# Kernel optimization log

Hardware: AMD Instinct MI355X
Metric: run time of the kernel (lower is better)

## Reference

```python
import jax, jax.numpy as jnp
import numpy as np

DIM = 1024
HEADS = 16
HEAD_DIM = DIM // HEADS  # 64
B, T, S = 4, 2048, 2048
NEG = -1e9


def rotary_pos_emb(x, freqs):
    # x: (B, H, L, Dh), freqs: (L, Dh//2). Rotate interleaved (even, odd) pairs.
    cos = jnp.cos(freqs)[None, None, :, :]  # (1,1,L,Dh//2)
    sin = jnp.sin(freqs)[None, None, :, :]
    x_even = x[..., 0::2]
    x_odd = x[..., 1::2]
    r_even = x_even * cos - x_odd * sin
    r_odd = x_even * sin + x_odd * cos
    return jnp.stack([r_even, r_odd], axis=-1).reshape(x.shape)


def setup_inputs() -> dict:
    key = jax.random.key(0)
    ks = jax.random.split(key, 9)
    w_std = 1.0 / np.sqrt(DIM)
    return {
        "q_x": jax.random.normal(ks[0], (B, T, DIM), jnp.float32),
        "kv_x": jax.random.normal(ks[1], (B, S, DIM), jnp.float32),
        "freq_q": jax.random.normal(ks[2], (T, HEAD_DIM // 2), jnp.float32),
        "freq_kv": jax.random.normal(ks[3], (S, HEAD_DIM // 2), jnp.float32),
        "key_padding_mask": jax.random.randint(ks[4], (B, S), 0, 2, jnp.int32),
        "Wq": jax.random.normal(ks[5], (DIM, DIM), jnp.float32) * w_std,
        "Wk": jax.random.normal(ks[6], (DIM, DIM), jnp.float32) * w_std,
        "Wv": jax.random.normal(ks[7], (DIM, DIM), jnp.float32) * w_std,
        "Wproj": jax.random.normal(ks[8], (DIM, DIM), jnp.float32) * w_std,
    }


def reference(q_x, kv_x, freq_q, freq_kv, key_padding_mask, Wq, Wk, Wv, Wproj):
    b, t, d = q_x.shape
    s = kv_x.shape[1]
    # QKV projections (torch Linear: x @ W.T), split into heads -> (B, H, L, Dh)
    q = (q_x @ Wq.T).reshape(b, t, HEADS, HEAD_DIM).transpose(0, 2, 1, 3)
    k = (kv_x @ Wk.T).reshape(b, s, HEADS, HEAD_DIM).transpose(0, 2, 1, 3)
    v = (kv_x @ Wv.T).reshape(b, s, HEADS, HEAD_DIM).transpose(0, 2, 1, 3)
    # Rotary embedding on q and k
    q = rotary_pos_emb(q, freq_q)
    k = rotary_pos_emb(k, freq_kv)
    # Scaled dot-product attention with key-padding mask (True = attend)
    scale = HEAD_DIM ** (-0.5)
    scores = jnp.einsum('bhtd,bhsd->bhts', q, k) * scale
    mask = key_padding_mask.astype(bool)[:, None, None, :]  # (B,1,1,S)
    scores = jnp.where(mask, scores, NEG)
    attn = jax.nn.softmax(scores, axis=-1)
    out = jnp.einsum('bhts,bhsd->bhtd', attn, v)
    out = out.transpose(0, 2, 1, 3).reshape(b, t, d)
    return out @ Wproj.T
```

## Files before the change

### kernel.cpp

```cpp
#include <hip/hip_runtime.h>
#include <hip/hip_bf16.h>


typedef __bf16 bf16;
typedef __bf16 bf16x8 __attribute__((ext_vector_type(8)));
typedef __bf16 bf16x4 __attribute__((ext_vector_type(4)));
typedef float  f32x4  __attribute__((ext_vector_type(4)));

#define NB   4
#define NT   2048
#define NS   2048
#define NH   16
#define HD   64
#define SCL  0.18033688011112043f

__device__ __forceinline__ void gload16(const void* g, void* l) {
  __builtin_amdgcn_global_load_lds((const __attribute__((address_space(1))) void*)g,
                                   (__attribute__((address_space(3))) void*)l, 16, 0, 0);
}

__device__ __forceinline__ f32x4 mfma16(bf16x8 a, bf16x8 b, f32x4 c) {
  return __builtin_amdgcn_mfma_f32_16x16x32_bf16(a, b, c, 0, 0, 0);
}

__global__ void k_convert(const float* __restrict__ qx, const float* __restrict__ kvx,
                          const float* __restrict__ Wq, const float* __restrict__ Wk,
                          const float* __restrict__ Wv, const float* __restrict__ Wp,
                          bf16* __restrict__ wbf, bf16* __restrict__ qxbf,
                          bf16* __restrict__ kvxbf)
{
  const long total = 4194304L + 8388608L + 8388608L;
  for (long v = (long)blockIdx.x * blockDim.x + threadIdx.x; v * 4 < total;
       v += (long)gridDim.x * blockDim.x) {
    long e0 = v * 4;
    const float* src; bf16* dst;
    if (e0 < 4194304L) {
      int widx = (int)(e0 >> 20);
      const float* wsrc = (widx == 0) ? Wq : (widx == 1) ? Wk : (widx == 2) ? Wv : Wp;
      src = wsrc + (e0 & 1048575); dst = wbf + e0;
    } else if (e0 < 12582912L) {
      src = qx + (e0 - 4194304L); dst = qxbf + (e0 - 4194304L);
    } else {
      src = kvx + (e0 - 12582912L); dst = kvxbf + (e0 - 12582912L);
    }
    float4 f = *(const float4*)src;
    bf16x4 o = {(bf16)f.x, (bf16)f.y, (bf16)f.z, (bf16)f.w};
    *(bf16x4*)dst = o;
  }
}

__global__ void k_tables(const float* __restrict__ fq, const float* __restrict__ fkv,
                         const int* __restrict__ mask,
                         float2* __restrict__ csq, float2* __restrict__ cskv,
                         float* __restrict__ bias)
{
  int i = blockIdx.x * blockDim.x + threadIdx.x;
  if (i < 65536) {
    float s, c; sincosf(fq[i], &s, &c); csq[i] = make_float2(c, s);
  } else if (i < 131072) {
    int j = i - 65536;
    float s, c; sincosf(fkv[j], &s, &c); cskv[j] = make_float2(c, s);
  } else if (i < 139264) {
    int j = i - 131072;
    bias[j] = mask[j] ? 0.0f : -1.0e9f;
  }
}

template<int EPI>
__global__ __launch_bounds__(256) void k_gemm(
    const bf16* __restrict__ A0, const bf16* __restrict__ A1,
    const bf16* __restrict__ wbase,
    bf16* __restrict__ Qb, bf16* __restrict__ Kb, bf16* __restrict__ Vtb,
    float* __restrict__ Of,
    const float2* __restrict__ csq, const float2* __restrict__ cskv)
{
  __shared__ bf16 As[128 * 32];
  __shared__ bf16 Bs[128 * 32];
  const int z  = (EPI == 0) ? blockIdx.z : 0;
  const bf16* A = (EPI == 1) ? A0 : ((z == 0) ? A0 : A1);
  const bf16* W = wbase + (size_t)z * 1048576;
  const int m0 = blockIdx.x * 128, n0 = blockIdx.y * 128;
  const int tid = threadIdx.x, lane = tid & 63, w = tid >> 6;
  const int g = lane >> 4, c = lane & 15;
  const int wr = w >> 1, wc = w & 1;

  f32x4 acc[4][4];
#pragma unroll
  for (int i = 0; i < 4; ++i)
#pragma unroll
    for (int j = 0; j < 4; ++j) acc[i][j] = 0.0f;

  const bf16* gA = A + (size_t)(m0 + w * 32 + (lane >> 2)) * 1024 + (lane & 3) * 8;
  const bf16* gB = W + (size_t)(n0 + w * 32 + (lane >> 2)) * 1024 + (lane & 3) * 8;
  bf16* lA = As + w * 1024;
  bf16* lB = Bs + w * 1024;

  for (int k0 = 0; k0 < 1024; k0 += 32) {
    __syncthreads();
    gload16(gA, lA);               gload16(gA + 16 * 1024, lA + 512);
    gload16(gB, lB);               gload16(gB + 16 * 1024, lB + 512);
    gA += 32; gB += 32;
    __syncthreads();

    bf16x8 af[4], bfr[4];
#pragma unroll
    for (int mi = 0; mi < 4; ++mi)
      af[mi] = *(const bf16x8*)(As + (wr * 64 + mi * 16 + c) * 32 + g * 8);
#pragma unroll
    for (int ni = 0; ni < 4; ++ni)
      bfr[ni] = *(const bf16x8*)(Bs + (wc * 64 + ni * 16 + c) * 32 + g * 8);
#pragma unroll
    for (int mi = 0; mi < 4; ++mi)
#pragma unroll
      for (int ni = 0; ni < 4; ++ni)
        acc[mi][ni] = mfma16(af[mi], bfr[ni], acc[mi][ni]);
  }

  if (EPI == 1) {
#pragma unroll
    for (int mi = 0; mi < 4; ++mi)
#pragma unroll
      for (int ni = 0; ni < 4; ++ni)
#pragma unroll
        for (int r = 0; r < 4; ++r) {
          int m = m0 + wr * 64 + mi * 16 + g * 4 + r;
          int n = n0 + wc * 64 + ni * 16 + c;
          Of[(size_t)m * 1024 + n] = acc[mi][ni][r];
        }
  } else if (z < 2) {
    const float2* cs = (z == 0) ? csq : cskv;
    bf16* Out = (z == 0) ? Qb : Kb;
#pragma unroll
    for (int mi = 0; mi < 4; ++mi)
#pragma unroll
      for (int ni = 0; ni < 4; ++ni)
#pragma unroll
        for (int r = 0; r < 4; ++r) {
          int m = m0 + wr * 64 + mi * 16 + g * 4 + r;
          int n = n0 + wc * 64 + ni * 16 + c;
          float v = acc[mi][ni][r];
          float p = __shfl_xor(v, 1);
          int t = m & 2047, b = m >> 11;
          int h = n >> 6, d = n & 63;
          float2 cv = cs[t * 32 + (d >> 1)];
          float rot = (d & 1) ? (v * cv.x + p * cv.y)
                              : (v * cv.x - p * cv.y);
          Out[((size_t)((b * 16 + h) * 2048 + t)) * 64 + d] = (bf16)rot;
        }
  } else {
#pragma unroll
    for (int mi = 0; mi < 4; ++mi)
#pragma unroll
      for (int ni = 0; ni < 4; ++ni) {
        int m = m0 + wr * 64 + mi * 16 + g * 4;
        int n = n0 + wc * 64 + ni * 16 + c;
        int b = m >> 11, sl = m & 2047;
        int h = n >> 6, d = n & 63;
        int p  = sl & 63;
        int st = p >> 4, q4 = (p >> 2) & 3;
        int col = (sl & ~63) | ((st >> 1) << 5) | (q4 << 3) | ((st & 1) << 2);
        bf16x4 pk = {(bf16)acc[mi][ni][0], (bf16)acc[mi][ni][1],
                     (bf16)acc[mi][ni][2], (bf16)acc[mi][ni][3]};
        *(bf16x4*)(Vtb + ((size_t)((b * 16 + h) * 64 + d)) * 2048 + col) = pk;
      }
  }
}

__global__ __launch_bounds__(256) void k_attn(
    const bf16* __restrict__ Qb, const bf16* __restrict__ Kb,
    const bf16* __restrict__ Vtb, const float* __restrict__ bias,
    bf16* __restrict__ Ob)
{
  __shared__ bf16 Ks[2][64 * 64];
  __shared__ bf16 Vs[2][80 * 64];
  __shared__ float Bls[2048];
  const int bh = blockIdx.y, b = bh >> 4, h = bh & 15;
  const int t0 = blockIdx.x * 128;
  const int tid = threadIdx.x, lane = tid & 63, w = tid >> 6;
  const int g = lane >> 4, c = lane & 15;

  {
    int rr = tid >> 4;
    int col4 = (tid & 15) * 4;
    bf16 v = (rr == 0) ? (bf16)1.0f : (bf16)0.0f;
    bf16x4 vv = {v, v, v, v};
    *(bf16x4*)(&Vs[0][(64 + rr) * 64 + col4]) = vv;
    *(bf16x4*)(&Vs[1][(64 + rr) * 64 + col4]) = vv;
  }
  {
    const float* bsrc = bias + b * 2048;
    float4 b0 = *(const float4*)(bsrc + tid * 4);
    float4 b1 = *(const float4*)(bsrc + 1024 + tid * 4);
    *(float4*)(&Bls[tid * 4]) = b0;
    *(float4*)(&Bls[1024 + tid * 4]) = b1;
  }

  bf16x8 qf[2][2];
#pragma unroll
  for (int qt = 0; qt < 2; ++qt) {
    const bf16* qp = Qb + ((size_t)bh * 2048 + t0 + qt * 64 + w * 16 + c) * 64;
    qf[qt][0] = *(const bf16x8*)(qp + g * 8);
    qf[qt][1] = *(const bf16x8*)(qp + 32 + g * 8);
  }

  float mrun[2] = {-3.0e38f, -3.0e38f};
  f32x4 o[2][5];
#pragma unroll
  for (int qt = 0; qt < 2; ++qt)
#pragma unroll
    for (int ni = 0; ni < 5; ++ni) o[qt][ni] = 0.0f;

  const int srow8 = lane >> 3;
  const int scol  = ((lane & 7) ^ srow8) * 8;
  const bf16* gK = Kb  + ((size_t)bh * 2048 + w * 16 + srow8) * 64 + scol;
  const bf16* gV = Vtb + ((size_t)bh * 64 + w * 16 + srow8) * 2048 + scol;

#define STAGE(bufi, ti)  do {                                   \
    const bf16* k_ = gK + ((size_t)(ti) << 12);                 \
    const bf16* v_ = gV + (size_t)(ti) * 64;                    \
    bf16* lk_ = &Ks[bufi][w * 1024];                            \
    bf16* lv_ = &Vs[bufi][w * 1024];                            \
    gload16(k_, lk_);            gload16(k_ + 512,      lk_ + 512); \
    gload16(v_, lv_);            gload16(v_ + 8 * 2048, lv_ + 512); \
  } while (0)

  STAGE(0, 0);
  asm volatile("s_waitcnt vmcnt(0)" ::: "memory");
  __syncthreads();

  for (int ti = 0; ti < 32; ++ti) {
    const int cur = ti & 1;
    if (ti < 31) STAGE(cur ^ 1, ti + 1);

    const bf16* KsC = Ks[cur];
    const bf16* VsC = Vs[cur];

    f32x4 sc[2][4];
#pragma unroll
    for (int qt = 0; qt < 2; ++qt)
#pragma unroll
      for (int st = 0; st < 4; ++st) sc[qt][st] = 0.0f;
    __builtin_amdgcn_s_setprio(1);
#pragma unroll
    for (int kd = 0; kd < 2; ++kd)
#pragma unroll
      for (int st = 0; st < 4; ++st) {
        int srow = st * 16 + c;
        bf16x8 kf = *(const bf16x8*)(KsC + srow * 64 + ((kd * 4 + g) ^ (srow & 7)) * 8);
        sc[0][st] = mfma16(kf, qf[0][kd], sc[0][st]);
        sc[1][st] = mfma16(kf, qf[1][kd], sc[1][st]);
      }
    __builtin_amdgcn_s_setprio(0);

    float4 bv[4];
#pragma unroll
    for (int st = 0; st < 4; ++st)
      bv[st] = *(const float4*)(&Bls[ti * 64 + st * 16 + g * 4]);

    bf16x8 pf[2][2];
#pragma unroll
    for (int qt = 0; qt < 2; ++qt) {
      float sv[4][4];
#pragma unroll
      for (int st = 0; st < 4; ++st)
#pragma unroll
        for (int r = 0; r < 4; ++r)
          sv[st][r] = sc[qt][st][r] * SCL + ((const float*)&bv[st])[r];

      float mt = sv[0][0];
#pragma unroll
      for (int st = 0; st < 4; ++st)
#pragma unroll
        for (int r = 0; r < 4; ++r) mt = fmaxf(mt, sv[st][r]);
      mt = fmaxf(mt, __shfl_xor(mt, 16));
      mt = fmaxf(mt, __shfl_xor(mt, 32));

      if (__any(mt > mrun[qt] + 8.0f)) {
        float mnew = fmaxf(mrun[qt], mt);
        float corr = exp2f(mrun[qt] - mnew);
        mrun[qt] = mnew;
#pragma unroll
        for (int ni = 0; ni < 5; ++ni) o[qt][ni] *= corr;
      }
#pragma unroll
      for (int ks = 0; ks < 2; ++ks)
#pragma unroll
        for (int st2 = 0; st2 < 2; ++st2) {
          int st = ks * 2 + st2;
#pragma unroll
          for (int r = 0; r < 4; ++r)
            pf[qt][ks][st2 * 4 + r] = (bf16)exp2f(sv[st][r] - mrun[qt]);
        }
    }

    __builtin_amdgcn_s_setprio(1);
#pragma unroll
    for (int ks = 0; ks < 2; ++ks)
#pragma unroll
      for (int ni = 0; ni < 5; ++ni) {
        int vrow = ni * 16 + c;
        bf16x8 vf = *(const bf16x8*)(VsC + vrow * 64 + (((ks * 4 + g) ^ (vrow & 7)) * 8));
        o[0][ni] = mfma16(vf, pf[0][ks], o[0][ni]);
        o[1][ni] = mfma16(vf, pf[1][ks], o[1][ni]);
      }
    __builtin_amdgcn_s_setprio(0);

    asm volatile("s_waitcnt vmcnt(0) lgkmcnt(0)" ::: "memory");
    __builtin_amdgcn_s_barrier();
  }
#undef STAGE

#pragma unroll
  for (int qt = 0; qt < 2; ++qt) {
    float l = __shfl(o[qt][4][0], c);
    float rl = 1.0f / l;
    int t = t0 + qt * 64 + w * 16 + c;
#pragma unroll
    for (int ni = 0; ni < 4; ++ni) {
      bf16x4 ov = {(bf16)(o[qt][ni][0] * rl), (bf16)(o[qt][ni][1] * rl),
                   (bf16)(o[qt][ni][2] * rl), (bf16)(o[qt][ni][3] * rl)};
      *(bf16x4*)(Ob + ((size_t)(b * 2048 + t)) * 1024 + h * 64 + ni * 16 + g * 4) = ov;
    }
  }
}

extern "C" void kernel_launch(void* const* d_in, const int* in_sizes, int n_in,
                              void* d_out, int out_size, void* d_ws, size_t ws_size,
                              hipStream_t stream)
{
  const float* qx  = (const float*)d_in[0];
  const float* kvx = (const float*)d_in[1];
  const float* fq  = (const float*)d_in[2];
  const float* fkv = (const float*)d_in[3];
  const int*  mask = (const int*)  d_in[4];
  const float* Wq  = (const float*)d_in[5];
  const float* Wk  = (const float*)d_in[6];
  const float* Wv  = (const float*)d_in[7];
  const float* Wp  = (const float*)d_in[8];

  char* ws = (char*)d_ws;
  bf16*   wbf   = (bf16*)(ws);
  bf16*   qxbf  = (bf16*)(ws + 8388608);
  bf16*   kvxbf = (bf16*)(ws + 25165824);
  bf16*   Qb    = (bf16*)(ws + 41943040);
  bf16*   Kb    = (bf16*)(ws + 58720256);
  bf16*   Vtb   = (bf16*)(ws + 75497472);
  bf16*   Ob    = (bf16*)(ws + 92274688);
  float2* csq   = (float2*)(ws + 109051904);
  float2* cskv  = (float2*)(ws + 109576192);
  float*  bias  = (float*)(ws + 110100480);
  float*  out   = (float*)d_out;

  k_convert<<<4096, 256, 0, stream>>>(qx, kvx, Wq, Wk, Wv, Wp, wbf, qxbf, kvxbf);
  k_tables<<<544, 256, 0, stream>>>(fq, fkv, mask, csq, cskv, bias);
  k_gemm<0><<<dim3(64, 8, 3), 256, 0, stream>>>(qxbf, kvxbf, wbf,
                                                Qb, Kb, Vtb, nullptr, csq, cskv);
  k_attn<<<dim3(16, 64), 256, 0, stream>>>(Qb, Kb, Vtb, bias, Ob);
  k_gemm<1><<<dim3(64, 8, 1), 256, 0, stream>>>(Ob, nullptr, wbf + 3 * 1048576,
                                                nullptr, nullptr, nullptr, out, csq, cskv);
}
```

Measured before the change: 380.5 us.

## Overlap K/V prefetch in attention, shrink LDS with bf16 bias, remap blocks per XCD

The attention kernel now waits only for the current tile's loads (vmcnt(4)) and adds a barrier before compute, so the next tile's global-to-LDS prefetch stays in flight during the compute. It also stores the key-padding bias as bf16 and moves the ones-row used for the softmax denominator into a separate small LDS buffer, which cuts shared memory use and may allow more resident blocks. Block indices are remapped so blocks for the same batch-head land on the same XCD, aiming for better L2 reuse of K/V. The bf16 bias keeps 0 and about -1e9 close enough to their fp32 values, and the extra barrier per iteration adds some synchronisation cost.

```diff
diff --git a/kernel.cpp b/kernel.cpp
--- a/kernel.cpp
+++ b/kernel.cpp
@@ -52,7 +52,7 @@
 __global__ void k_tables(const float* __restrict__ fq, const float* __restrict__ fkv,
                          const int* __restrict__ mask,
                          float2* __restrict__ csq, float2* __restrict__ cskv,
-                         float* __restrict__ bias)
+                         float* __restrict__ bias, bf16* __restrict__ biasbf)
 {
   int i = blockIdx.x * blockDim.x + threadIdx.x;
   if (i < 65536) {
@@ -63,6 +63,9 @@
   } else if (i < 139264) {
     int j = i - 131072;
     bias[j] = mask[j] ? 0.0f : -1.0e9f;
+  } else if (i < 147456) {
+    int j = i - 139264;
+    biasbf[j] = mask[j] ? (bf16)0.0f : (bf16)(-1.0e9f);
   }
 }
 
@@ -168,14 +171,18 @@
 
 __global__ __launch_bounds__(256) void k_attn(
     const bf16* __restrict__ Qb, const bf16* __restrict__ Kb,
-    const bf16* __restrict__ Vtb, const float* __restrict__ bias,
+    const bf16* __restrict__ Vtb, const bf16* __restrict__ biasbf,
     bf16* __restrict__ Ob)
 {
   __shared__ bf16 Ks[2][64 * 64];
-  __shared__ bf16 Vs[2][80 * 64];
-  __shared__ float Bls[2048];
-  const int bh = blockIdx.y, b = bh >> 4, h = bh & 15;
-  const int t0 = blockIdx.x * 128;
+  __shared__ bf16 Vs[2][64 * 64];
+  __shared__ bf16 Vones[16 * 64];
+  __shared__ bf16 Blsb[2048];
+  const int lin = blockIdx.y * 16 + blockIdx.x;
+  const int xcd = lin & 7, j = lin >> 3;
+  const int bh = xcd * 8 + (j >> 4);
+  const int t0 = (j & 15) * 128;
+  const int b = bh >> 4, h = bh & 15;
   const int tid = threadIdx.x, lane = tid & 63, w = tid >> 6;
   const int g = lane >> 4, c = lane & 15;
 
@@ -184,16 +191,9 @@
     int col4 = (tid & 15) * 4;
     bf16 v = (rr == 0) ? (bf16)1.0f : (bf16)0.0f;
     bf16x4 vv = {v, v, v, v};
-    *(bf16x4*)(&Vs[0][(64 + rr) * 64 + col4]) = vv;
-    *(bf16x4*)(&Vs[1][(64 + rr) * 64 + col4]) = vv;
-  }
-  {
-    const float* bsrc = bias + b * 2048;
-    float4 b0 = *(const float4*)(bsrc + tid * 4);
-    float4 b1 = *(const float4*)(bsrc + 1024 + tid * 4);
-    *(float4*)(&Bls[tid * 4]) = b0;
-    *(float4*)(&Bls[1024 + tid * 4]) = b1;
-  }
+    *(bf16x4*)(&Vones[rr * 64 + col4]) = vv;
+  }
+  bf16x8 bb0 = *(const bf16x8*)(biasbf + b * 2048 + tid * 8);
 
   bf16x8 qf[2][2];
 #pragma unroll
@@ -202,6 +202,7 @@
     qf[qt][0] = *(const bf16x8*)(qp + g * 8);
     qf[qt][1] = *(const bf16x8*)(qp + 32 + g * 8);
   }
+  *(bf16x8*)(&Blsb[tid * 8]) = bb0;
 
   float mrun[2] = {-3.0e38f, -3.0e38f};
   f32x4 o[2][5];
@@ -225,12 +226,18 @@
   } while (0)
 
   STAGE(0, 0);
-  asm volatile("s_waitcnt vmcnt(0)" ::: "memory");
-  __syncthreads();
+  asm volatile("s_waitcnt vmcnt(0) lgkmcnt(0)" ::: "memory");
+  __builtin_amdgcn_s_barrier();
 
   for (int ti = 0; ti < 32; ++ti) {
     const int cur = ti & 1;
-    if (ti < 31) STAGE(cur ^ 1, ti + 1);
+    if (ti < 31) {
+      STAGE(cur ^ 1, ti + 1);
+      asm volatile("s_waitcnt vmcnt(4)" ::: "memory");
+    } else {
+      asm volatile("s_waitcnt vmcnt(0)" ::: "memory");
+    }
+    __builtin_amdgcn_s_barrier();
 
     const bf16* KsC = Ks[cur];
     const bf16* VsC = Vs[cur];
@@ -252,10 +259,10 @@
       }
     __builtin_amdgcn_s_setprio(0);
 
-    float4 bv[4];
+    bf16x4 bv[4];
 #pragma unroll
     for (int st = 0; st < 4; ++st)
-      bv[st] = *(const float4*)(&Bls[ti * 64 + st * 16 + g * 4]);
+      bv[st] = *(const bf16x4*)(&Blsb[ti * 64 + st * 16 + g * 4]);
 
     bf16x8 pf[2][2];
 #pragma unroll
@@ -265,7 +272,7 @@
       for (int st = 0; st < 4; ++st)
 #pragma unroll
         for (int r = 0; r < 4; ++r)
-          sv[st][r] = sc[qt][st][r] * SCL + ((const float*)&bv[st])[r];
+          sv[st][r] = sc[qt][st][r] * SCL + (float)bv[st][r];
 
       float mt = sv[0][0];
 #pragma unroll
@@ -298,14 +305,14 @@
     for (int ks = 0; ks < 2; ++ks)
 #pragma unroll
       for (int ni = 0; ni < 5; ++ni) {
-        int vrow = ni * 16 + c;
-        bf16x8 vf = *(const bf16x8*)(VsC + vrow * 64 + (((ks * 4 + g) ^ (vrow & 7)) * 8));
+        const bf16* vbase = (ni < 4) ? (VsC + (ni * 16 + c) * 64) : (Vones + c * 64);
+        bf16x8 vf = *(const bf16x8*)(vbase + (((ks * 4 + g) ^ (c & 7)) * 8));
         o[0][ni] = mfma16(vf, pf[0][ks], o[0][ni]);
         o[1][ni] = mfma16(vf, pf[1][ks], o[1][ni]);
       }
     __builtin_amdgcn_s_setprio(0);
 
-    asm volatile("s_waitcnt vmcnt(0) lgkmcnt(0)" ::: "memory");
+    asm volatile("s_waitcnt lgkmcnt(0)" ::: "memory");
     __builtin_amdgcn_s_barrier();
   }
 #undef STAGE
@@ -339,23 +346,24 @@
   const float* Wp  = (const float*)d_in[8];
 
   char* ws = (char*)d_ws;
-  bf16*   wbf   = (bf16*)(ws);
-  bf16*   qxbf  = (bf16*)(ws + 8388608);
-  bf16*   kvxbf = (bf16*)(ws + 25165824);
-  bf16*   Qb    = (bf16*)(ws + 41943040);
-  bf16*   Kb    = (bf16*)(ws + 58720256);
-  bf16*   Vtb   = (bf16*)(ws + 75497472);
-  bf16*   Ob    = (bf16*)(ws + 92274688);
-  float2* csq   = (float2*)(ws + 109051904);
-  float2* cskv  = (float2*)(ws + 109576192);
-  float*  bias  = (float*)(ws + 110100480);
-  float*  out   = (float*)d_out;
+  bf16*   wbf    = (bf16*)(ws);
+  bf16*   qxbf   = (bf16*)(ws + 8388608);
+  bf16*   kvxbf  = (bf16*)(ws + 25165824);
+  bf16*   Qb     = (bf16*)(ws + 41943040);
+  bf16*   Kb     = (bf16*)(ws + 58720256);
+  bf16*   Vtb    = (bf16*)(ws + 75497472);
+  bf16*   Ob     = (bf16*)(ws + 92274688);
+  float2* csq    = (float2*)(ws + 109051904);
+  float2* cskv   = (float2*)(ws + 109576192);
+  float*  bias   = (float*)(ws + 110100480);
+  bf16*   biasbf = (bf16*)(ws + 110133248);
+  float*  out    = (float*)d_out;
 
   k_convert<<<4096, 256, 0, stream>>>(qx, kvx, Wq, Wk, Wv, Wp, wbf, qxbf, kvxbf);
-  k_tables<<<544, 256, 0, stream>>>(fq, fkv, mask, csq, cskv, bias);
+  k_tables<<<576, 256, 0, stream>>>(fq, fkv, mask, csq, cskv, bias, biasbf);
   k_gemm<0><<<dim3(64, 8, 3), 256, 0, stream>>>(qxbf, kvxbf, wbf,
                                                 Qb, Kb, Vtb, nullptr, csq, cskv);
-  k_attn<<<dim3(16, 64), 256, 0, stream>>>(Qb, Kb, Vtb, bias, Ob);
+  k_attn<<<dim3(16, 64), 256, 0, stream>>>(Qb, Kb, Vtb, biasbf, Ob);
   k_gemm<1><<<dim3(64, 8, 1), 256, 0, stream>>>(Ob, nullptr, wbf + 3 * 1048576,
                                                 nullptr, nullptr, nullptr, out, csq, cskv);
 }
```

New measurement: 380.7 us. Within noise of the previous version (+0.1%).
